# Kernel optimization log

Hardware: AMD Instinct MI355X
Metric: run time of the kernel (lower is better)

Reference implementation:

```python
import jax, jax.numpy as jnp
import numpy as np
from jax import lax

T = 128          # max_length
C_EXPLORE = 10.0 # tanh_exploration
NEG_INF = -1e30  # stand-in for -inf (safe under fp32 softmax)


def setup_inputs() -> dict:
    key = jax.random.key(0)
    ks = jax.random.split(key, 19)
    B, S, E, H = 512, 256, 128, 128
    sc = 0.05
    return {
        "decoder_input": jax.random.normal(ks[0], (B, E), jnp.float32),
        "embedded_inputs": jax.random.normal(ks[1], (S, B, E), jnp.float32),
        "h0": jax.random.normal(ks[2], (B, H), jnp.float32),
        "c0": jax.random.normal(ks[3], (B, H), jnp.float32),
        "context": jax.random.normal(ks[4], (S, B, H), jnp.float32),
        "Wi": jax.random.normal(ks[5], (4 * H, E), jnp.float32) * sc,
        "bi": jax.random.normal(ks[6], (4 * H,), jnp.float32) * sc,
        "Wh": jax.random.normal(ks[7], (4 * H, H), jnp.float32) * sc,
        "bh": jax.random.normal(ks[8], (4 * H,), jnp.float32) * sc,
        "Wq_g": jax.random.normal(ks[9], (H, H), jnp.float32) * sc,
        "bq_g": jax.random.normal(ks[10], (H,), jnp.float32) * sc,
        "Wref_g": jax.random.normal(ks[11], (H, H), jnp.float32) * sc,
        "bref_g": jax.random.normal(ks[12], (H,), jnp.float32) * sc,
        "v_g": jax.random.normal(ks[13], (H,), jnp.float32) * sc,
        "Wq_p": jax.random.normal(ks[14], (H, H), jnp.float32) * sc,
        "bq_p": jax.random.normal(ks[15], (H,), jnp.float32) * sc,
        "Wref_p": jax.random.normal(ks[16], (H, H), jnp.float32) * sc,
        "bref_p": jax.random.normal(ks[17], (H,), jnp.float32) * sc,
        "v_p": jax.random.normal(ks[18], (H,), jnp.float32) * sc,
    }


def _apply_mask(logits, mask, prev_idxs, has_prev):
    # torch: maskk[b, prev]=1; maskk[b,0]=0; logits[maskk]=-inf (only if prev_idxs given)
    B = logits.shape[0]
    m2 = mask.at[jnp.arange(B), prev_idxs].set(True).at[:, 0].set(False)
    m2 = jnp.where(has_prev, m2, mask)
    return jnp.where(m2, NEG_INF, logits), m2


def reference(decoder_input, embedded_inputs, h0, c0, context,
              Wi, bi, Wh, bh,
              Wq_g, bq_g, Wref_g, bref_g, v_g,
              Wq_p, bq_p, Wref_p, bref_p, v_p):
    S, B, E = embedded_inputs.shape
    # conv1d(kernel=1) over fixed context: precompute once (identical math each step)
    e_g = jnp.einsum('oh,sbh->bso', Wref_g, context) + bref_g  # [B,S,H]
    e_p = jnp.einsum('oh,sbh->bso', Wref_p, context) + bref_p  # [B,S,H]
    keys = jax.random.split(jax.random.key(42), T)

    def step(carry, key):
        dec_in, hx, cx, mask, prev, has_prev, finished = carry
        # LSTM cell
        gates = dec_in @ Wi.T + bi + hx @ Wh.T + bh  # [B,4H]
        ig, fg, cg, og = jnp.split(gates, 4, axis=1)
        cy = jax.nn.sigmoid(fg) * cx + jax.nn.sigmoid(ig) * jnp.tanh(cg)
        hy = jax.nn.sigmoid(og) * jnp.tanh(cy)
        # glimpse attention (n_glimpses=1, no tanh clip)
        q = hy @ Wq_g.T + bq_g                                   # [B,H]
        u = jnp.einsum('h,bsh->bs', v_g, jnp.tanh(q[:, None, :] + e_g))
        u, mask = _apply_mask(u, mask, prev, has_prev)
        a = jax.nn.softmax(u, axis=-1)                           # [B,S]
        g_l = jnp.einsum('bsh,bs->bh', e_g, a)                   # bmm(ref, probs)
        # pointer attention with tanh exploration
        q = g_l @ Wq_p.T + bq_p
        u = jnp.einsum('h,bsh->bs', v_p, jnp.tanh(q[:, None, :] + e_p))
        logits = C_EXPLORE * jnp.tanh(u)
        logits, mask = _apply_mask(logits, mask, prev, has_prev)
        probs = jax.nn.softmax(logits, axis=-1)
        # categorical sample from probs == categorical over masked logits
        idx = jax.random.categorical(key, logits).astype(jnp.int32)
        idx = idx * finished
        finished = finished * (idx != 0).astype(jnp.int32)
        dec_in_new = embedded_inputs[idx, jnp.arange(B), :]      # [B,E]
        new_carry = (dec_in_new, hy, cy, mask, idx, jnp.array(True), finished)
        return new_carry, (probs, idx)

    carry0 = (decoder_input, h0, c0,
              jnp.zeros((B, S), bool), jnp.zeros((B,), jnp.int32),
              jnp.array(False), jnp.ones((B,), jnp.int32))
    (_, hx, cx, _, _, _, _), (probs, sels) = lax.scan(step, carry0, keys)
    return probs, sels, hx, cx  # probs [T,B,S], sels [T,B]
```

## Files before the change

kernel.cpp:

```cpp
#include <hip/hip_runtime.h>
#include <stdint.h>

#define BB 512
#define SS 256
#define EE 128
#define HH 128
#define TT 128
#define G4 512

#define NEG_INF_F (-1e30f)
#define TINY_F32  1.17549435e-38f

typedef float v2f __attribute__((ext_vector_type(2)));

__device__ __forceinline__ uint32_t rotl32(uint32_t v, int r){ return (v<<r)|(v>>(32-r)); }

__device__ __forceinline__ void threefry2x32(uint32_t k0, uint32_t k1,
                                             uint32_t c0, uint32_t c1,
                                             uint32_t* o0, uint32_t* o1){
  uint32_t ks2 = k0 ^ k1 ^ 0x1BD11BDAu;
  uint32_t x0 = c0 + k0;
  uint32_t x1 = c1 + k1;
#define TF_R(rr) { x0 += x1; x1 = rotl32(x1, rr); x1 ^= x0; }
  TF_R(13) TF_R(15) TF_R(26) TF_R(6)
  x0 += k1; x1 += ks2 + 1u;
  TF_R(17) TF_R(29) TF_R(16) TF_R(24)
  x0 += ks2; x1 += k0 + 2u;
  TF_R(13) TF_R(15) TF_R(26) TF_R(6)
  x0 += k0; x1 += k1 + 3u;
  TF_R(17) TF_R(29) TF_R(16) TF_R(24)
  x0 += k1; x1 += ks2 + 4u;
  TF_R(13) TF_R(15) TF_R(26) TF_R(6)
  x0 += ks2; x1 += k0 + 5u;
#undef TF_R
  *o0 = x0; *o1 = x1;
}

__device__ __forceinline__ float xla_tanhf(float x){
#pragma clang fp contract(off)
  float ax = fabsf(x);
  float xc = fminf(fmaxf(x, -9.0f), 9.0f);
  float x2 = xc*xc;
  float num = -2.76076847742355e-16f;
  num = x2*num + 2.00018790482477e-13f;
  num = x2*num + -8.60467152213735e-11f;
  num = x2*num + 5.12229709037114e-08f;
  num = x2*num + 1.48572235717979e-05f;
  num = x2*num + 6.37261928875436e-04f;
  num = x2*num + 4.89352455891786e-03f;
  num = xc*num;
  float den = 1.19825839466702e-06f;
  den = x2*den + 1.18534705686654e-04f;
  den = x2*den + 2.26843463243900e-03f;
  den = x2*den + 4.89352518554385e-03f;
  return (ax < 4e-4f) ? x : (num/den);
}

__device__ __forceinline__ float xla_sigmoidf(float x){
#pragma clang fp contract(off)
  return 0.5f + 0.5f * xla_tanhf(0.5f * x);
}

__device__ __forceinline__ v2f splat2(float c){ v2f r; r.x = c; r.y = c; return r; }

__device__ __forceinline__ v2f xla_tanh2(v2f x){
#pragma clang fp contract(off)
  v2f xc;
  xc.x = fminf(fmaxf(x.x, -9.0f), 9.0f);
  xc.y = fminf(fmaxf(x.y, -9.0f), 9.0f);
  v2f x2 = xc*xc;
  v2f num = splat2(-2.76076847742355e-16f);
  num = x2*num + splat2( 2.00018790482477e-13f);
  num = x2*num + splat2(-8.60467152213735e-11f);
  num = x2*num + splat2( 5.12229709037114e-08f);
  num = x2*num + splat2( 1.48572235717979e-05f);
  num = x2*num + splat2( 6.37261928875436e-04f);
  num = x2*num + splat2( 4.89352455891786e-03f);
  num = xc*num;
  v2f den = splat2( 1.19825839466702e-06f);
  den = x2*den + splat2( 1.18534705686654e-04f);
  den = x2*den + splat2( 2.26843463243900e-03f);
  den = x2*den + splat2( 4.89352518554385e-03f);
  v2f r;
  r.x = num.x/den.x;
  r.y = num.y/den.y;
  r.x = (fabsf(x.x) < 4e-4f) ? x.x : r.x;
  r.y = (fabsf(x.y) < 4e-4f) ? x.y : r.y;
  return r;
}

__device__ __forceinline__ void quad_acc(double& acc, const float4 q, const float4 g,
                                         float e0, float e1, float e2, float e3){
#pragma clang fp contract(off)
  v2f a; a.x = q.x + e0; a.y = q.y + e1;
  v2f t = xla_tanh2(a);
  acc += (double)g.x * (double)t.x;
  acc += (double)g.y * (double)t.y;
  v2f b; b.x = q.z + e2; b.y = q.w + e3;
  v2f u = xla_tanh2(b);
  acc += (double)g.z * (double)u.x;
  acc += (double)g.w * (double)u.y;
}

__device__ __forceinline__ double wave_sum_f64(double v){
  #pragma unroll
  for (int off = 32; off; off >>= 1) v += __shfl_xor(v, off, 64);
  return v;
}

__global__ __launch_bounds__(256) void precompute_e_kernel(
    const float* __restrict__ ctx, const float* __restrict__ W,
    const float* __restrict__ bias, float* __restrict__ e_out)
{
#pragma clang fp contract(off)
  __shared__ float Ct[64][65];
  __shared__ float Wt[128][65];
  const int tid = threadIdx.x;
  const int tx = tid & 31;
  const int ty = tid >> 5;
  const size_t r0 = (size_t)blockIdx.x * 64;

  double acc[8][4];
  #pragma unroll
  for (int i=0;i<8;++i){
    #pragma unroll
    for (int j=0;j<4;++j) acc[i][j]=0.0;
  }

  for (int kc=0; kc<2; ++kc){
    for (int idx = tid; idx < 64*64; idx += 256){
      const int row = idx >> 6, col = idx & 63;
      Ct[row][col] = ctx[(r0 + row)*HH + kc*64 + col];
    }
    for (int idx = tid; idx < 128*64; idx += 256){
      const int row = idx >> 6, col = idx & 63;
      Wt[row][col] = W[row*HH + kc*64 + col];
    }
    __syncthreads();
    #pragma unroll 4
    for (int kk=0; kk<64; ++kk){
      float cv[8], wv[4];
      #pragma unroll
      for (int i=0;i<8;++i) cv[i] = Ct[ty + 8*i][kk];
      #pragma unroll
      for (int j=0;j<4;++j) wv[j] = Wt[tx + 32*j][kk];
      #pragma unroll
      for (int i=0;i<8;++i){
        #pragma unroll
        for (int j=0;j<4;++j) acc[i][j] += (double)cv[i] * (double)wv[j];
      }
    }
    __syncthreads();
  }
  #pragma unroll
  for (int i=0;i<8;++i){
    const size_t r = r0 + ty + 8*i;
    const int s  = (int)(r >> 9);
    const int bb = (int)(r & 511);
    float* dst = e_out + ((size_t)bb*SS + s)*HH;
    #pragma unroll
    for (int j=0;j<4;++j){
      const int c = tx + 32*j;
      dst[c] = (float)acc[i][j] + bias[c];
    }
  }
}

__global__ void pack_weights_kernel(
    const float* __restrict__ Wi, const float* __restrict__ Wh,
    const float* __restrict__ Wqg, const float* __restrict__ Wqp,
    float* __restrict__ WiP, float* __restrict__ WhP,
    float* __restrict__ WqgP, float* __restrict__ WqpP)
{
  const int i = blockIdx.x * blockDim.x + threadIdx.x;
  if (i < G4*EE){
    const int j = i / EE, e = i % EE;
    const size_t d = ((size_t)(e>>2)*G4 + j)*4 + (e&3);
    WiP[d] = Wi[i];
    WhP[d] = Wh[i];
  }
  if (i < HH*HH){
    const int o = i / HH, k = i % HH;
    const size_t d = ((size_t)(k>>2)*HH + o)*4 + (k&3);
    WqgP[d] = Wqg[i];
    WqpP[d] = Wqp[i];
  }
}

__global__ __launch_bounds__(1024, 4) void decode_kernel(
    const float* __restrict__ dec0, const float* __restrict__ h0v, const float* __restrict__ c0v,
    const float* __restrict__ WiP, const float* __restrict__ WhP,
    const float* __restrict__ bi, const float* __restrict__ bh,
    const float* __restrict__ WqgP, const float* __restrict__ bqg, const float* __restrict__ vg,
    const float* __restrict__ WqpP, const float* __restrict__ bqp, const float* __restrict__ vp,
    const float* __restrict__ e_g, const float* __restrict__ e_p,
    const float* __restrict__ emb,
    float* __restrict__ probs_out, float* __restrict__ sels_out,
    float* __restrict__ hx_out, float* __restrict__ cx_out)
{
#pragma clang fp contract(off)
  const int b = blockIdx.x;
  const int tid = threadIdx.x;
  const int lane = tid & 63;
  const int w = tid >> 6;

  __shared__ float  e_s[SS][HH];
  __shared__ double parts8[8][258];
  __shared__ float  u_s[SS];
  __shared__ float  gates_s[G4];
  __shared__ float  dec_s[EE], hy_s[HH], c_s[HH], gl_s[HH];
  __shared__ float  q4_s[4][132];
  __shared__ float  vg4_s[4][132];
  __shared__ float  vp4_s[4][132];
  __shared__ float  bqg_s[HH], bqp_s[HH];
  __shared__ uint32_t keys0_s[TT], keys1_s[TT];
  __shared__ unsigned char mask_s[SS];
  __shared__ float  fred_s[4];
  __shared__ double dred_s[4];
  __shared__ float  amax_v[4];
  __shared__ int    amax_i[4];
  __shared__ int    idx_sh, fin_sh;

  const float* egb = e_g + (size_t)b*SS*HH;
  const float* epb = e_p + (size_t)b*SS*HH;

  if (tid < HH){
    dec_s[tid] = dec0[b*EE + tid];
    hy_s[tid]  = h0v[b*HH + tid];
    c_s[tid]   = c0v[b*HH + tid];
    const float vgv = vg[tid];
    const float vpv = vp[tid];
    #pragma unroll
    for (int c=0;c<4;++c){ vg4_s[c][tid] = vgv; vp4_s[c][tid] = vpv; }
    bqg_s[tid] = bqg[tid];
    bqp_s[tid] = bqp[tid];
  }
  if (tid < SS) mask_s[tid] = 0;
  if (tid < TT){
    uint32_t kk0, kk1;
    threefry2x32(0u, 42u, 0u, (uint32_t)tid, &kk0, &kk1);
    keys0_s[tid] = kk0; keys1_s[tid] = kk1;
  }
  if (tid == 0) fin_sh = 1;
  for (int idx = tid; idx < SS*32; idx += 1024){
    const int r  = idx >> 5;
    const int c4 = (idx & 31) << 2;
    *(float4*)&e_s[r][c4] = ((const float4*)egb)[idx];
  }
  __syncthreads();

  const int sD = tid >> 2;
  const int q4r = tid & 3;
  float eD[32], eG[32];
  #pragma unroll
  for (int i=0;i<32;++i) eD[i] = e_s[sD][q4r*32 + i];
  {
    const float4* epr = (const float4*)(epb + sD*HH + q4r*32);
    #pragma unroll
    for (int k=0;k<8;++k) *(float4*)&eG[4*k] = epr[k];
  }

  for (int t = 0; t < TT; ++t){
    double* aux = &parts8[0][0];
    double a0 = 0.0;
    if (tid < 512){
      const float4* Wp = (const float4*)WiP + tid;
      double p0=0.0,p1=0.0,p2=0.0,p3=0.0;
      #pragma unroll 8
      for (int e4=0;e4<32;++e4){
        const float4 wv = Wp[(size_t)e4*G4];
        const float4 dv = *(const float4*)&dec_s[e4*4];
        p0 += (double)dv.x * (double)wv.x;
        p1 += (double)dv.y * (double)wv.y;
        p2 += (double)dv.z * (double)wv.z;
        p3 += (double)dv.w * (double)wv.w;
      }
      a0 = ((p0+p1)+p2)+p3;
    } else {
      const int j = tid - 512;
      const float4* Wp = (const float4*)WhP + j;
      double r0=0.0,r1=0.0,r2=0.0,r3=0.0;
      #pragma unroll 8
      for (int k4=0;k4<32;++k4){
        const float4 wv = Wp[(size_t)k4*G4];
        const float4 hv = *(const float4*)&hy_s[k4*4];
        r0 += (double)hv.x * (double)wv.x;
        r1 += (double)hv.y * (double)wv.y;
        r2 += (double)hv.z * (double)wv.z;
        r3 += (double)hv.w * (double)wv.w;
      }
      aux[j] = ((r0+r1)+r2)+r3;
    }
    __syncthreads();
    if (tid < 512){
      const int j = tid;
      const float g = (float)a0 + bi[j] + (float)aux[j] + bh[j];
      gates_s[j] = ((j >> 7) == 2) ? xla_tanhf(g) : xla_sigmoidf(g);
    }
    __syncthreads();

    if (tid < HH){
      const int h = tid;
      const float cn = gates_s[HH+h]*c_s[h] + gates_s[h]*gates_s[2*HH+h];
      const float hn = gates_s[3*HH+h]*xla_tanhf(cn);
      c_s[h] = cn; hy_s[h] = hn;
    }
    __syncthreads();

    if (tid < 512){
      const int o = tid & 127, qc = tid >> 7;
      const float4* Wc = (const float4*)WqgP + (size_t)qc*8*HH + o;
      double acc = 0.0;
      #pragma unroll
      for (int i8=0;i8<8;++i8){
        const float4 wv = Wc[(size_t)i8*HH];
        const float4 hv = *(const float4*)&hy_s[qc*32 + i8*4];
        acc += (double)hv.x * (double)wv.x;
        acc += (double)hv.y * (double)wv.y;
        acc += (double)hv.z * (double)wv.z;
        acc += (double)hv.w * (double)wv.w;
      }
      parts8[qc][o] = acc;
    }
    __syncthreads();
    if (tid < HH){
      const float qq = (float)(((parts8[0][tid]+parts8[1][tid])+parts8[2][tid])+parts8[3][tid]) + bqg_s[tid];
      #pragma unroll
      for (int c=0;c<4;++c) q4_s[c][tid] = qq;
    }
    __syncthreads();

    const bool skipRow = (mask_s[sD] != 0);
    if (!skipRow){
      #pragma unroll
      for (int cc=0; cc<2; ++cc){
        const int hb = q4r*32 + cc*16;
        const float4 qa = *(const float4*)&q4_s[q4r][hb+0];
        const float4 qb = *(const float4*)&q4_s[q4r][hb+4];
        const float4 qc4= *(const float4*)&q4_s[q4r][hb+8];
        const float4 qd = *(const float4*)&q4_s[q4r][hb+12];
        const float4 ga = *(const float4*)&vg4_s[q4r][hb+0];
        const float4 gb = *(const float4*)&vg4_s[q4r][hb+4];
        const float4 gc = *(const float4*)&vg4_s[q4r][hb+8];
        const float4 gd = *(const float4*)&vg4_s[q4r][hb+12];
        const int eb = cc*16;
        double acc = 0.0;
        quad_acc(acc, qa, ga, eD[eb+0],  eD[eb+1],  eD[eb+2],  eD[eb+3]);
        quad_acc(acc, qb, gb, eD[eb+4],  eD[eb+5],  eD[eb+6],  eD[eb+7]);
        quad_acc(acc, qc4,gc, eD[eb+8],  eD[eb+9],  eD[eb+10], eD[eb+11]);
        quad_acc(acc, qd, gd, eD[eb+12], eD[eb+13], eD[eb+14], eD[eb+15]);
        parts8[q4r*2 + cc][sD] = acc;
      }
    }
    __syncthreads();

    if (tid < SS){
      float uf;
      if (mask_s[tid]) uf = NEG_INF_F;
      else {
        double u = 0.0;
        #pragma unroll
        for (int wi=0;wi<8;++wi) u += parts8[wi][tid];
        uf = (float)u;
      }
      u_s[tid] = uf;
    }
    __syncthreads();

    {
      float x = 0.0f;
      if (tid < SS){
        x = u_s[tid];
        float wm = x;
        #pragma unroll
        for (int off=32; off; off>>=1) wm = fmaxf(wm, __shfl_xor(wm, off, 64));
        if (lane == 0) fred_s[w] = wm;
      }
      __syncthreads();
      const float m = fmaxf(fmaxf(fred_s[0], fred_s[1]), fmaxf(fred_s[2], fred_s[3]));
      float p = 0.0f;
      if (tid < SS){
        p = mask_s[tid] ? 0.0f : expf(x - m);
        const double zs = wave_sum_f64((double)p);
        if (lane == 0) dred_s[w] = zs;
      }
      __syncthreads();
      const float Z = (float)(dred_s[0] + dred_s[1] + dred_s[2] + dred_s[3]);
      if (tid < SS) u_s[tid] = p / Z;
    }
    __syncthreads();

    {
      const int h = tid & 127, p8 = tid >> 7;
      double acc = 0.0;
      #pragma unroll
      for (int g4i=0; g4i<8; ++g4i){
        const int s0 = p8*32 + g4i*4;
        const float4 uv = *(const float4*)&u_s[s0];
        acc += (double)uv.x * (double)e_s[s0+0][h];
        acc += (double)uv.y * (double)e_s[s0+1][h];
        acc += (double)uv.z * (double)e_s[s0+2][h];
        acc += (double)uv.w * (double)e_s[s0+3][h];
      }
      parts8[p8][h] = acc;
    }
    __syncthreads();
    if (tid < HH){
      double g = parts8[0][tid];
      #pragma unroll
      for (int p8=1;p8<8;++p8) g += parts8[p8][tid];
      gl_s[tid] = (float)g;
    }
    __syncthreads();

    if (tid < 512){
      const int o = tid & 127, qc = tid >> 7;
      const float4* Wc = (const float4*)WqpP + (size_t)qc*8*HH + o;
      double acc = 0.0;
      #pragma unroll
      for (int i8=0;i8<8;++i8){
        const float4 wv = Wc[(size_t)i8*HH];
        const float4 hv = *(const float4*)&gl_s[qc*32 + i8*4];
        acc += (double)hv.x * (double)wv.x;
        acc += (double)hv.y * (double)wv.y;
        acc += (double)hv.z * (double)wv.z;
        acc += (double)hv.w * (double)wv.w;
      }
      parts8[qc][o] = acc;
    }
    __syncthreads();
    if (tid < HH){
      const float qq = (float)(((parts8[0][tid]+parts8[1][tid])+parts8[2][tid])+parts8[3][tid]) + bqp_s[tid];
      #pragma unroll
      for (int c=0;c<4;++c) q4_s[c][tid] = qq;
    }
    __syncthreads();

    if (!skipRow){
      #pragma unroll
      for (int cc=0; cc<2; ++cc){
        const int hb = q4r*32 + cc*16;
        const float4 qa = *(const float4*)&q4_s[q4r][hb+0];
        const float4 qb = *(const float4*)&q4_s[q4r][hb+4];
        const float4 qc4= *(const float4*)&q4_s[q4r][hb+8];
        const float4 qd = *(const float4*)&q4_s[q4r][hb+12];
        const float4 ga = *(const float4*)&vp4_s[q4r][hb+0];
        const float4 gb = *(const float4*)&vp4_s[q4r][hb+4];
        const float4 gc = *(const float4*)&vp4_s[q4r][hb+8];
        const float4 gd = *(const float4*)&vp4_s[q4r][hb+12];
        const int eb = cc*16;
        double acc = 0.0;
        quad_acc(acc, qa, ga, eG[eb+0],  eG[eb+1],  eG[eb+2],  eG[eb+3]);
        quad_acc(acc, qb, gb, eG[eb+4],  eG[eb+5],  eG[eb+6],  eG[eb+7]);
        quad_acc(acc, qc4,gc, eG[eb+8],  eG[eb+9],  eG[eb+10], eG[eb+11]);
        quad_acc(acc, qd, gd, eG[eb+12], eG[eb+13], eG[eb+14], eG[eb+15]);
        parts8[q4r*2 + cc][sD] = acc;
      }
    }
    __syncthreads();

    float logit_x = NEG_INF_F;
    if (tid < SS){
      if (!mask_s[tid]){
        double u = 0.0;
        #pragma unroll
        for (int wi=0;wi<8;++wi) u += parts8[wi][tid];
        logit_x = 10.0f * xla_tanhf((float)u);
      }
    }

    {
      const float x = logit_x;
      if (tid < SS){
        float wm = x;
        #pragma unroll
        for (int off=32; off; off>>=1) wm = fmaxf(wm, __shfl_xor(wm, off, 64));
        if (lane == 0) fred_s[w] = wm;
      }
      __syncthreads();
      const float m = fmaxf(fmaxf(fred_s[0], fred_s[1]), fmaxf(fred_s[2], fred_s[3]));
      float p = 0.0f;
      if (tid < SS){
        p = mask_s[tid] ? 0.0f : expf(x - m);
        const double zs = wave_sum_f64((double)p);
        if (lane == 0) dred_s[w] = zs;
      }
      __syncthreads();
      const float Z = (float)(dred_s[0] + dred_s[1] + dred_s[2] + dred_s[3]);
      if (tid < SS) probs_out[((size_t)t*BB + b)*SS + tid] = p / Z;
    }

    {
      if (tid < SS){
        float y = -3.0e38f;
        if (!mask_s[tid]){
          uint32_t r0, r1;
          threefry2x32(keys0_s[t], keys1_s[t], 0u, (uint32_t)(b*SS + tid), &r0, &r1);
          const uint32_t bits = r0 ^ r1;
          const float f = __uint_as_float((bits >> 9) | 0x3f800000u) - 1.0f;
          const float u01 = fmaxf(TINY_F32, f);
          const float g = -logf(-logf(u01));
          y = logit_x + g;
        }
        int bi_ = tid;
        #pragma unroll
        for (int off=32; off; off>>=1){
          const float oy = __shfl_xor(y, off, 64);
          const int oi = __shfl_xor(bi_, off, 64);
          if (oy > y || (oy == y && oi < bi_)){ y = oy; bi_ = oi; }
        }
        if (lane == 0){ amax_v[w] = y; amax_i[w] = bi_; }
      }
      __syncthreads();
      if (tid == 0){
        float bv = amax_v[0]; int bidx = amax_i[0];
        #pragma unroll
        for (int k=1;k<4;++k){
          if (amax_v[k] > bv || (amax_v[k] == bv && amax_i[k] < bidx)){ bv = amax_v[k]; bidx = amax_i[k]; }
        }
        const int fin = fin_sh;
        const int idx = fin ? bidx : 0;
        sels_out[(size_t)t*BB + b] = (float)idx;
        fin_sh = (fin && idx != 0) ? 1 : 0;
        mask_s[idx] = 1;
        mask_s[0] = 0;
        idx_sh = idx;
      }
      __syncthreads();
      if (tid < EE){
        dec_s[tid] = emb[((size_t)idx_sh*BB + b)*EE + tid];
      }
    }
    __syncthreads();
  }

  if (tid < HH){
    hx_out[b*HH + tid] = hy_s[tid];
    cx_out[b*HH + tid] = c_s[tid];
  }
}

__global__ void ws_fail_kernel(float* sels_out){
  if (threadIdx.x == 0 && blockIdx.x == 0) sels_out[0] = -77777.0f;
}

extern "C" void kernel_launch(void* const* d_in, const int* in_sizes, int n_in,
                              void* d_out, int out_size, void* d_ws, size_t ws_size,
                              hipStream_t stream)
{
  const float* decoder_input = (const float*)d_in[0];
  const float* embedded      = (const float*)d_in[1];
  const float* h0            = (const float*)d_in[2];
  const float* c0            = (const float*)d_in[3];
  const float* context       = (const float*)d_in[4];
  const float* Wi            = (const float*)d_in[5];
  const float* bi            = (const float*)d_in[6];
  const float* Wh            = (const float*)d_in[7];
  const float* bh            = (const float*)d_in[8];
  const float* Wq_g          = (const float*)d_in[9];
  const float* bq_g          = (const float*)d_in[10];
  const float* Wref_g        = (const float*)d_in[11];
  const float* bref_g        = (const float*)d_in[12];
  const float* v_g           = (const float*)d_in[13];
  const float* Wq_p          = (const float*)d_in[14];
  const float* bq_p          = (const float*)d_in[15];
  const float* Wref_p        = (const float*)d_in[16];
  const float* bref_p        = (const float*)d_in[17];
  const float* v_p           = (const float*)d_in[18];

  char* ws = (char*)d_ws;
  size_t off = 0;
  auto alloc = [&](size_t bytes) -> void* {
    void* p = ws + off;
    off += (bytes + 255) & ~(size_t)255;
    return p;
  };
  float* e_g  = (float*)alloc((size_t)BB*SS*HH*4);
  float* e_p  = (float*)alloc((size_t)BB*SS*HH*4);
  float* WiP  = (float*)alloc((size_t)EE*G4*4);
  float* WhP  = (float*)alloc((size_t)HH*G4*4);
  float* WqgP = (float*)alloc((size_t)HH*HH*4);
  float* WqpP = (float*)alloc((size_t)HH*HH*4);

  float* probs_out = (float*)d_out;
  float* sels_out  = probs_out + (size_t)TT*BB*SS;
  float* hx_out    = sels_out + (size_t)TT*BB;
  float* cx_out    = hx_out + (size_t)BB*HH;

  if (off > ws_size){
    ws_fail_kernel<<<1, 64, 0, stream>>>(sels_out);
    return;
  }

  pack_weights_kernel<<<(G4*EE + 255)/256, 256, 0, stream>>>(
      Wi, Wh, Wq_g, Wq_p, WiP, WhP, WqgP, WqpP);
  precompute_e_kernel<<<(SS*BB)/64, 256, 0, stream>>>(context, Wref_g, bref_g, e_g);
  precompute_e_kernel<<<(SS*BB)/64, 256, 0, stream>>>(context, Wref_p, bref_p, e_p);

  decode_kernel<<<BB, 1024, 0, stream>>>(
      decoder_input, h0, c0,
      WiP, WhP, bi, bh,
      WqgP, bq_g, v_g,
      WqpP, bq_p, v_p,
      e_g, e_p, embedded,
      probs_out, sels_out, hx_out, cx_out);
}
```

Measured before the change: 9.975 ms.

## Swizzle e_s shared layout, remap rows per thread, drop eD registers

Stores e_g in shared memory with an XOR swizzle on float4 columns and remaps threads so each wave covers consecutive rows (sD = tid&255), with each thread loading its 32-element slice from shared memory every step instead of keeping eD in registers. With that mapping a whole wave reads the same part of q and v, so the replicated q4/vg4/vp4 arrays become plain q_s/vg_s/vp_s. It also merges the u_s store with the max reduction, removing one barrier. The aims are fewer LDS bank conflicts, less register pressure and one fewer sync per step, at the cost of extra shared-memory reads per step.

```diff
diff --git a/kernel.cpp b/kernel.cpp
--- a/kernel.cpp
+++ b/kernel.cpp
@@ -209,9 +209,7 @@
   __shared__ float  u_s[SS];
   __shared__ float  gates_s[G4];
   __shared__ float  dec_s[EE], hy_s[HH], c_s[HH], gl_s[HH];
-  __shared__ float  q4_s[4][132];
-  __shared__ float  vg4_s[4][132];
-  __shared__ float  vp4_s[4][132];
+  __shared__ float  q_s[HH], vg_s[HH], vp_s[HH];
   __shared__ float  bqg_s[HH], bqp_s[HH];
   __shared__ uint32_t keys0_s[TT], keys1_s[TT];
   __shared__ unsigned char mask_s[SS];
@@ -228,10 +226,8 @@
     dec_s[tid] = dec0[b*EE + tid];
     hy_s[tid]  = h0v[b*HH + tid];
     c_s[tid]   = c0v[b*HH + tid];
-    const float vgv = vg[tid];
-    const float vpv = vp[tid];
-    #pragma unroll
-    for (int c=0;c<4;++c){ vg4_s[c][tid] = vgv; vp4_s[c][tid] = vpv; }
+    vg_s[tid]  = vg[tid];
+    vp_s[tid]  = vp[tid];
     bqg_s[tid] = bqg[tid];
     bqp_s[tid] = bqp[tid];
   }
@@ -244,21 +240,22 @@
   if (tid == 0) fin_sh = 1;
   for (int idx = tid; idx < SS*32; idx += 1024){
     const int r  = idx >> 5;
-    const int c4 = (idx & 31) << 2;
-    *(float4*)&e_s[r][c4] = ((const float4*)egb)[idx];
+    const int c4 = idx & 31;
+    *(float4*)&e_s[r][(c4 ^ (r & 7)) << 2] = ((const float4*)egb)[idx];
   }
   __syncthreads();
 
-  const int sD = tid >> 2;
-  const int q4r = tid & 3;
-  float eD[32], eG[32];
-  #pragma unroll
-  for (int i=0;i<32;++i) eD[i] = e_s[sD][q4r*32 + i];
+  const int sD  = tid & 255;
+  const int q4r = tid >> 8;
+  float eG[32];
   {
     const float4* epr = (const float4*)(epb + sD*HH + q4r*32);
     #pragma unroll
     for (int k=0;k<8;++k) *(float4*)&eG[4*k] = epr[k];
   }
+  const int hE  = tid & 127;
+  const int p8E = tid >> 7;
+  const int h4E = hE >> 2, hmE = hE & 3;
 
   for (int t = 0; t < TT; ++t){
     double* aux = &parts8[0][0];
@@ -323,64 +320,60 @@
       parts8[qc][o] = acc;
     }
     __syncthreads();
-    if (tid < HH){
-      const float qq = (float)(((parts8[0][tid]+parts8[1][tid])+parts8[2][tid])+parts8[3][tid]) + bqg_s[tid];
-      #pragma unroll
-      for (int c=0;c<4;++c) q4_s[c][tid] = qq;
-    }
+    if (tid < HH)
+      q_s[tid] = (float)(((parts8[0][tid]+parts8[1][tid])+parts8[2][tid])+parts8[3][tid]) + bqg_s[tid];
     __syncthreads();
 
     const bool skipRow = (mask_s[sD] != 0);
     if (!skipRow){
+      float ev[32];
+      #pragma unroll
+      for (int m=0;m<8;++m){
+        const int c4 = ((q4r<<3) + m) ^ (sD & 7);
+        *(float4*)&ev[m*4] = *(const float4*)&e_s[sD][c4<<2];
+      }
       #pragma unroll
       for (int cc=0; cc<2; ++cc){
         const int hb = q4r*32 + cc*16;
-        const float4 qa = *(const float4*)&q4_s[q4r][hb+0];
-        const float4 qb = *(const float4*)&q4_s[q4r][hb+4];
-        const float4 qc4= *(const float4*)&q4_s[q4r][hb+8];
-        const float4 qd = *(const float4*)&q4_s[q4r][hb+12];
-        const float4 ga = *(const float4*)&vg4_s[q4r][hb+0];
-        const float4 gb = *(const float4*)&vg4_s[q4r][hb+4];
-        const float4 gc = *(const float4*)&vg4_s[q4r][hb+8];
-        const float4 gd = *(const float4*)&vg4_s[q4r][hb+12];
+        const float4 qa = *(const float4*)&q_s[hb+0];
+        const float4 qb = *(const float4*)&q_s[hb+4];
+        const float4 qc4= *(const float4*)&q_s[hb+8];
+        const float4 qd = *(const float4*)&q_s[hb+12];
+        const float4 ga = *(const float4*)&vg_s[hb+0];
+        const float4 gb = *(const float4*)&vg_s[hb+4];
+        const float4 gc = *(const float4*)&vg_s[hb+8];
+        const float4 gd = *(const float4*)&vg_s[hb+12];
         const int eb = cc*16;
         double acc = 0.0;
-        quad_acc(acc, qa, ga, eD[eb+0],  eD[eb+1],  eD[eb+2],  eD[eb+3]);
-        quad_acc(acc, qb, gb, eD[eb+4],  eD[eb+5],  eD[eb+6],  eD[eb+7]);
-        quad_acc(acc, qc4,gc, eD[eb+8],  eD[eb+9],  eD[eb+10], eD[eb+11]);
-        quad_acc(acc, qd, gd, eD[eb+12], eD[eb+13], eD[eb+14], eD[eb+15]);
+        quad_acc(acc, qa, ga, ev[eb+0],  ev[eb+1],  ev[eb+2],  ev[eb+3]);
+        quad_acc(acc, qb, gb, ev[eb+4],  ev[eb+5],  ev[eb+6],  ev[eb+7]);
+        quad_acc(acc, qc4,gc, ev[eb+8],  ev[eb+9],  ev[eb+10], ev[eb+11]);
+        quad_acc(acc, qd, gd, ev[eb+12], ev[eb+13], ev[eb+14], ev[eb+15]);
         parts8[q4r*2 + cc][sD] = acc;
       }
     }
     __syncthreads();
 
+    float x1 = 0.0f;
     if (tid < SS){
-      float uf;
-      if (mask_s[tid]) uf = NEG_INF_F;
+      if (mask_s[tid]) x1 = NEG_INF_F;
       else {
         double u = 0.0;
         #pragma unroll
         for (int wi=0;wi<8;++wi) u += parts8[wi][tid];
-        uf = (float)u;
-      }
-      u_s[tid] = uf;
-    }
-    __syncthreads();
-
+        x1 = (float)u;
+      }
+      float wm = x1;
+      #pragma unroll
+      for (int off=32; off; off>>=1) wm = fmaxf(wm, __shfl_xor(wm, off, 64));
+      if (lane == 0) fred_s[w] = wm;
+    }
+    __syncthreads();
     {
-      float x = 0.0f;
-      if (tid < SS){
-        x = u_s[tid];
-        float wm = x;
-        #pragma unroll
-        for (int off=32; off; off>>=1) wm = fmaxf(wm, __shfl_xor(wm, off, 64));
-        if (lane == 0) fred_s[w] = wm;
-      }
-      __syncthreads();
       const float m = fmaxf(fmaxf(fred_s[0], fred_s[1]), fmaxf(fred_s[2], fred_s[3]));
       float p = 0.0f;
       if (tid < SS){
-        p = mask_s[tid] ? 0.0f : expf(x - m);
+        p = mask_s[tid] ? 0.0f : expf(x1 - m);
         const double zs = wave_sum_f64((double)p);
         if (lane == 0) dred_s[w] = zs;
       }
@@ -391,18 +384,17 @@
     __syncthreads();
 
     {
-      const int h = tid & 127, p8 = tid >> 7;
       double acc = 0.0;
       #pragma unroll
       for (int g4i=0; g4i<8; ++g4i){
-        const int s0 = p8*32 + g4i*4;
+        const int s0 = p8E*32 + g4i*4;
         const float4 uv = *(const float4*)&u_s[s0];
-        acc += (double)uv.x * (double)e_s[s0+0][h];
-        acc += (double)uv.y * (double)e_s[s0+1][h];
-        acc += (double)uv.z * (double)e_s[s0+2][h];
-        acc += (double)uv.w * (double)e_s[s0+3][h];
-      }
-      parts8[p8][h] = acc;
+        acc += (double)uv.x * (double)e_s[s0+0][((h4E ^ ((s0+0)&7))<<2) | hmE];
+        acc += (double)uv.y * (double)e_s[s0+1][((h4E ^ ((s0+1)&7))<<2) | hmE];
+        acc += (double)uv.z * (double)e_s[s0+2][((h4E ^ ((s0+2)&7))<<2) | hmE];
+        acc += (double)uv.w * (double)e_s[s0+3][((h4E ^ ((s0+3)&7))<<2) | hmE];
+      }
+      parts8[p8E][hE] = acc;
     }
     __syncthreads();
     if (tid < HH){
@@ -429,25 +421,22 @@
       parts8[qc][o] = acc;
     }
     __syncthreads();
-    if (tid < HH){
-      const float qq = (float)(((parts8[0][tid]+parts8[1][tid])+parts8[2][tid])+parts8[3][tid]) + bqp_s[tid];
-      #pragma unroll
-      for (int c=0;c<4;++c) q4_s[c][tid] = qq;
-    }
+    if (tid < HH)
+      q_s[tid] = (float)(((parts8[0][tid]+parts8[1][tid])+parts8[2][tid])+parts8[3][tid]) + bqp_s[tid];
     __syncthreads();
 
     if (!skipRow){
       #pragma unroll
       for (int cc=0; cc<2; ++cc){
         const int hb = q4r*32 + cc*16;
-        const float4 qa = *(const float4*)&q4_s[q4r][hb+0];
-        const float4 qb = *(const float4*)&q4_s[q4r][hb+4];
-        const float4 qc4= *(const float4*)&q4_s[q4r][hb+8];
-        const float4 qd = *(const float4*)&q4_s[q4r][hb+12];
-        const float4 ga = *(const float4*)&vp4_s[q4r][hb+0];
-        const float4 gb = *(const float4*)&vp4_s[q4r][hb+4];
-        const float4 gc = *(const float4*)&vp4_s[q4r][hb+8];
-        const float4 gd = *(const float4*)&vp4_s[q4r][hb+12];
+        const float4 qa = *(const float4*)&q_s[hb+0];
+        const float4 qb = *(const float4*)&q_s[hb+4];
+        const float4 qc4= *(const float4*)&q_s[hb+8];
+        const float4 qd = *(const float4*)&q_s[hb+12];
+        const float4 ga = *(const float4*)&vp_s[hb+0];
+        const float4 gb = *(const float4*)&vp_s[hb+4];
+        const float4 gc = *(const float4*)&vp_s[hb+8];
+        const float4 gd = *(const float4*)&vp_s[hb+12];
         const int eb = cc*16;
         double acc = 0.0;
         quad_acc(acc, qa, ga, eG[eb+0],  eG[eb+1],  eG[eb+2],  eG[eb+3]);
```

After: 8.203 ms. 17.8% less time.
